# Kernel optimization log

Measured on AMD Instinct MI355X. Metric: run time of the kernel, lower is better.

The kernel has to match this reference:

```python
import jax, jax.numpy as jnp
import numpy as np

TOP_K = 2
SCALING = 16.0 / 8.0  # alpha / rank


def setup_inputs() -> dict:
    key = jax.random.key(0)
    ks = jax.random.split(key, 9)
    B, V, D, P = 32, 21, 512, 64
    IN, OUT, E, R, H = D * P, 96, 8, 8, 256
    return {
        "x": jax.random.normal(ks[0], (B, V, D, P), jnp.float32),
        "W_base": jax.random.normal(ks[1], (OUT, IN), jnp.float32) * (IN ** -0.5),
        "b_base": jax.random.normal(ks[2], (OUT,), jnp.float32) * 0.01,
        "W1": jax.random.normal(ks[3], (H, D), jnp.float32) * (D ** -0.5),
        "b1": jax.random.normal(ks[4], (H,), jnp.float32) * 0.01,
        "W2": jax.random.normal(ks[5], (E, H), jnp.float32) * (H ** -0.5),
        "b2": jax.random.normal(ks[6], (E,), jnp.float32) * 0.01,
        "lora_A": jax.random.normal(ks[7], (E, R, IN), jnp.float32) * (IN ** -0.5),
        "lora_B": jax.random.normal(ks[8], (E, OUT, R), jnp.float32) * (R ** -0.5),
    }


def reference(x, W_base, b_base, W1, b1, W2, b2, lora_A, lora_B):
    B, V, D, P = x.shape
    E = lora_A.shape[0]
    # FlattenHead: flatten last two dims, then linear (dropout is identity in eval)
    flat = x.reshape(B, V, D * P)                      # [B, V, IN]
    base_out = flat @ W_base.T + b_base                # [B, V, OUT]
    # Router: pool over n_vars then patch dim -> [B, D]
    pooled = x.mean(axis=1).mean(axis=-1)
    h = jax.nn.relu(pooled @ W1.T + b1)
    logits = h @ W2.T + b2                             # [B, E]
    probs = jax.nn.softmax(logits, axis=-1)
    topw, topi = jax.lax.top_k(probs, TOP_K)           # [B, K]
    topw = topw / jnp.clip(topw.sum(-1, keepdims=True), 1e-6)
    # All LoRA experts (matches original dense compute), then weighted combine
    temp = jnp.einsum("bvi,eri->ebvr", flat, lora_A)   # [E, B, V, R]
    delta = jnp.einsum("ebvr,eor->ebvo", temp, lora_B) * SCALING  # [E, B, V, OUT]
    # Scatter top-k weights into dense [B, E] then combine (top-k sparse combine)
    w_full = jnp.zeros((B, E), x.dtype).at[jnp.arange(B)[:, None], topi].add(topw)
    moe_delta = jnp.einsum("be,ebvo->bvo", w_full, delta)
    return base_out + moe_delta, probs
```

## Files before the change

kernel.cpp:

```cpp
#include <hip/hip_runtime.h>

#define B_DIM 32
#define V_DIM 21
#define D_DIM 512
#define P_DIM 64
#define M_TOTAL 672
#define K_TOTAL 32768
#define OUT_DIM 96
#define E_DIM 8
#define R_DIM 8
#define H_DIM 256
#define N_TOTAL 160
#define SCALING 2.0f
#define POOL_SCALE (1.0f / (V_DIM * (float)P_DIM))

#define BM 64
#define BK 32
#define KSPLIT 32
#define K_PER_SPLIT (K_TOTAL / KSPLIT)
#define CHUNKS (K_PER_SPLIT / BK)
#define SMN (M_TOTAL * N_TOTAL)
#define NMB 11
#define RC_ROWS 4

typedef __attribute__((ext_vector_type(4))) float floatx4;
typedef __attribute__((ext_vector_type(8))) short short8;

__device__ __forceinline__ unsigned short f2bf(float f) {
  union { float f; unsigned int u; } v; v.f = f;
  unsigned int u = v.u + (0x7FFFu + ((v.u >> 16) & 1u));
  return (unsigned short)(u >> 16);
}

__device__ __forceinline__ unsigned int cvt_pk_bf16(float lo, float hi) {
  unsigned int r;
  asm("v_cvt_pk_bf16_f32 %0, %1, %2" : "=v"(r) : "v"(lo), "v"(hi));
  return r;
}

__device__ __forceinline__ void gl_lds16(const void* g, void* l) {
  __builtin_amdgcn_global_load_lds(
      (const __attribute__((address_space(1))) void*)g,
      (__attribute__((address_space(3))) void*)l, 16, 0, 0);
}

__device__ __forceinline__ short8 as_s8(floatx4 v) {
  union { floatx4 f; short8 s; } u; u.f = v; return u.s;
}

__global__ __launch_bounds__(256)
void convW_kernel(const float* __restrict__ W_base, const float* __restrict__ lora_A,
                  short* __restrict__ Wb) {
  int gid = blockIdx.x * 256 + threadIdx.x;
  size_t base = (size_t)gid * 8;
  int row = (int)(base >> 15);
  int k = (int)(base & 32767);
  const float* src = (row < OUT_DIM) ? (W_base + ((size_t)row << 15) + k)
                                     : (lora_A + ((size_t)(row - OUT_DIM) << 15) + k);
  floatx4 v0 = ((const floatx4*)src)[0];
  floatx4 v1 = ((const floatx4*)src)[1];
  short8 sv;
  sv[0] = (short)f2bf(v0[0]); sv[1] = (short)f2bf(v0[1]);
  sv[2] = (short)f2bf(v0[2]); sv[3] = (short)f2bf(v0[3]);
  sv[4] = (short)f2bf(v1[0]); sv[5] = (short)f2bf(v1[1]);
  sv[6] = (short)f2bf(v1[2]); sv[7] = (short)f2bf(v1[3]);
  *(short8*)(Wb + base) = sv;
}

__global__ __launch_bounds__(256, 2)
void gemm_kernel(const float* __restrict__ x, const short* __restrict__ Wb,
                 float* __restrict__ P, float* __restrict__ pp) {
  __shared__ __attribute__((aligned(16))) short ldsB[4][N_TOTAL * BK];
  __shared__ float lds_pool[5 * 16];

  const int tid = threadIdx.x;
  const int bid = blockIdx.x;
  const int xcd = bid & 7;
  const int grp = bid >> 3;
  const int ky  = xcd + 8 * (grp / NMB);
  const int mb  = grp % NMB;
  const int m0 = mb * BM;
  const int kbase = ky * K_PER_SPLIT;
  const int lane = tid & 63;
  const int wave = tid >> 6;
  const int quad = lane >> 4;
  const int l16 = lane & 15;
  const int b_first = m0 / V_DIM;

  if (tid < 80) lds_pool[tid] = 0.0f;
  asm volatile("s_waitcnt lgkmcnt(0)" ::: "memory");

  const int arow_raw = m0 + wave * 16 + l16;
  const bool row_ok = (arow_raw < M_TOTAL);
  const int arow = row_ok ? arow_raw : (M_TOTAL - 1);
  const floatx4* aptr =
      (const floatx4*)(x + (size_t)arow * K_TOTAL + kbase + quad * 8);

  const short* srcB0; const short* srcB1; const short* srcB2 = Wb;
  int dstB0, dstB1, dstB2 = 0;
  {
    int idx = tid, pair = idx >> 3, s8 = idx & 7;
    srcB0 = Wb + (size_t)(2 * pair + (s8 >> 2)) * K_TOTAL + kbase + (s8 & 3) * 8;
    dstB0 = (tid & 192) << 3;
    idx = 256 + tid; pair = idx >> 3; s8 = idx & 7;
    srcB1 = Wb + (size_t)(2 * pair + (s8 >> 2)) * K_TOTAL + kbase + (s8 & 3) * 8;
    dstB1 = (256 + (tid & 192)) << 3;
    if (tid < 128) {
      idx = 512 + tid; pair = idx >> 3; s8 = idx & 7;
      srcB2 = Wb + (size_t)(2 * pair + (s8 >> 2)) * K_TOTAL + kbase + (s8 & 3) * 8;
      dstB2 = (512 + (tid & 192)) << 3;
    }
  }
  const unsigned baddr =
      (unsigned)(size_t)(__attribute__((address_space(3))) short*)&ldsB[0][0] +
      (unsigned)((l16 >> 1) * 128 + ((((l16 & 1) << 2) | quad) * 16));

#define ISSUE_B(c, bb)                                                        \
  {                                                                           \
    gl_lds16(srcB0 + (c) * BK, &ldsB[bb][dstB0]);                             \
    gl_lds16(srcB1 + (c) * BK, &ldsB[bb][dstB1]);                             \
    if (tid < 128) gl_lds16(srcB2 + (c) * BK, &ldsB[bb][dstB2]);              \
  }
#define WAITV(N) asm volatile("s_waitcnt vmcnt(" #N ")" ::: "memory")
#define SBAR __builtin_amdgcn_sched_barrier(0)

  floatx4 af[4][2];
  floatx4 acc[10];
  #pragma unroll
  for (int nt = 0; nt < 10; ++nt) acc[nt] = (floatx4)(0.0f);
  floatx4 paccv = (floatx4)(0.0f);

  ISSUE_B(0, 0); SBAR;
  af[0][0] = aptr[0];  af[0][1] = aptr[1];  SBAR;
  ISSUE_B(1, 1); SBAR;
  af[1][0] = aptr[8];  af[1][1] = aptr[9];  SBAR;
  ISSUE_B(2, 2); SBAR;
  af[2][0] = aptr[16]; af[2][1] = aptr[17];
  af[3][0] = aptr[24]; af[3][1] = aptr[25];

  #pragma unroll
  for (int c = 0; c < CHUNKS; ++c) {
    const int bb = c & 3;
    if (c <= CHUNKS - 4)      { if (wave < 2) WAITV(12); else WAITV(10); }
    else if (c == CHUNKS - 3) { if (wave < 2) WAITV(10); else WAITV(8); }
    else if (c == CHUNKS - 2) { if (wave < 2) WAITV(5);  else WAITV(4); }
    else                      { WAITV(0); }
    SBAR;
    __builtin_amdgcn_s_barrier();
    SBAR;
    if (c + 3 < CHUNKS) ISSUE_B(c + 3, (c + 3) & 3);
    SBAR;
    floatx4 f0 = af[bb][0], f1 = af[bb][1];
    union { short8 s; unsigned int u[4]; } av;
    av.u[0] = cvt_pk_bf16(f0[0], f0[1]);
    av.u[1] = cvt_pk_bf16(f0[2], f0[3]);
    av.u[2] = cvt_pk_bf16(f1[0], f1[1]);
    av.u[3] = cvt_pk_bf16(f1[2], f1[3]);
    paccv += f0 + f1;
    if (c & 1) {
      float h = (paccv[0] + paccv[1]) + (paccv[2] + paccv[3]);
      h += __shfl_down(h, 32);
      h += __shfl_down(h, 16);
      if (lane < 16 && row_ok)
        atomicAdd(&lds_pool[(arow / V_DIM - b_first) * 16 + (c >> 1)], h);
      paccv = (floatx4)(0.0f);
    }
    if (c + 4 < CHUNKS) {
      af[bb][0] = aptr[(c + 4) * 8];
      af[bb][1] = aptr[(c + 4) * 8 + 1];
    }
    const unsigned ba = baddr + (unsigned)(bb * (N_TOTAL * BK * 2));
    floatx4 b0, b1, b2, b3, b4, b5, b6, b7, b8, b9;
    asm volatile("ds_read_b128 %0, %1 offset:0"    : "=&v"(b0) : "v"(ba));
    asm volatile("ds_read_b128 %0, %1 offset:1024" : "=&v"(b1) : "v"(ba));
    asm volatile("ds_read_b128 %0, %1 offset:2048" : "=&v"(b2) : "v"(ba));
    asm volatile("ds_read_b128 %0, %1 offset:3072" : "=&v"(b3) : "v"(ba));
    asm volatile("ds_read_b128 %0, %1 offset:4096" : "=&v"(b4) : "v"(ba));
    asm volatile("ds_read_b128 %0, %1 offset:5120" : "=&v"(b5) : "v"(ba));
    asm volatile("ds_read_b128 %0, %1 offset:6144" : "=&v"(b6) : "v"(ba));
    asm volatile("ds_read_b128 %0, %1 offset:7168" : "=&v"(b7) : "v"(ba));
    asm volatile("ds_read_b128 %0, %1 offset:8192" : "=&v"(b8) : "v"(ba));
    asm volatile("ds_read_b128 %0, %1 offset:9216" : "=&v"(b9) : "v"(ba));
    asm volatile("s_waitcnt lgkmcnt(0)" ::: "memory");
    SBAR;
    acc[0] = __builtin_amdgcn_mfma_f32_16x16x32_bf16(av.s, as_s8(b0), acc[0], 0, 0, 0);
    acc[1] = __builtin_amdgcn_mfma_f32_16x16x32_bf16(av.s, as_s8(b1), acc[1], 0, 0, 0);
    acc[2] = __builtin_amdgcn_mfma_f32_16x16x32_bf16(av.s, as_s8(b2), acc[2], 0, 0, 0);
    acc[3] = __builtin_amdgcn_mfma_f32_16x16x32_bf16(av.s, as_s8(b3), acc[3], 0, 0, 0);
    acc[4] = __builtin_amdgcn_mfma_f32_16x16x32_bf16(av.s, as_s8(b4), acc[4], 0, 0, 0);
    acc[5] = __builtin_amdgcn_mfma_f32_16x16x32_bf16(av.s, as_s8(b5), acc[5], 0, 0, 0);
    acc[6] = __builtin_amdgcn_mfma_f32_16x16x32_bf16(av.s, as_s8(b6), acc[6], 0, 0, 0);
    acc[7] = __builtin_amdgcn_mfma_f32_16x16x32_bf16(av.s, as_s8(b7), acc[7], 0, 0, 0);
    acc[8] = __builtin_amdgcn_mfma_f32_16x16x32_bf16(av.s, as_s8(b8), acc[8], 0, 0, 0);
    acc[9] = __builtin_amdgcn_mfma_f32_16x16x32_bf16(av.s, as_s8(b9), acc[9], 0, 0, 0);
  }

  __syncthreads();

  {
    const int mrow = m0 + wave * 16 + quad * 4;
    float* Pp = P + (size_t)ky * SMN + (size_t)mrow * N_TOTAL + l16;
    #pragma unroll
    for (int r = 0; r < 4; ++r)
      if (mrow + r < M_TOTAL)
        #pragma unroll
        for (int nt = 0; nt < 10; ++nt)
          Pp[(size_t)r * N_TOTAL + nt * 16] = acc[nt][r];
  }

  if (tid < 80) {
    int bl = tid >> 4, dl = tid & 15;
    pp[((size_t)(mb * 5 + bl)) * D_DIM + ky * 16 + dl] = lds_pool[tid];
  }
}

__global__ __launch_bounds__(256)
void router_kernel(const float* __restrict__ pp, const float* __restrict__ W1,
                   const float* __restrict__ b1, const float* __restrict__ W2,
                   const float* __restrict__ b2, float* __restrict__ wfull,
                   float* __restrict__ probs_out) {
  __shared__ float sp[D_DIM];
  __shared__ float sh[H_DIM];
  __shared__ float slog[E_DIM];
  const int b = blockIdx.x;
  const int t = threadIdx.x;
  const int mb1 = (b * V_DIM) / BM;
  const int mb2 = (b * V_DIM + V_DIM - 1) / BM;
  const int bf1 = (mb1 * BM) / V_DIM;
  const int bf2 = (mb2 * BM) / V_DIM;
  const float* p1 = pp + (size_t)(mb1 * 5 + (b - bf1)) * D_DIM;
  const float* p2 = pp + (size_t)(mb2 * 5 + (b - bf2)) * D_DIM;
  for (int d = t; d < D_DIM; d += 256) {
    float v = p1[d];
    if (mb2 != mb1) v += p2[d];
    sp[d] = v * POOL_SCALE;
  }
  __syncthreads();
  float acc = b1[t];
  const float* w1r = W1 + (size_t)t * D_DIM;
  for (int d = 0; d < D_DIM; ++d) acc += sp[d] * w1r[d];
  sh[t] = fmaxf(acc, 0.0f);
  __syncthreads();
  if (t < E_DIM) {
    float a = b2[t];
    const float* w2r = W2 + t * H_DIM;
    for (int j = 0; j < H_DIM; ++j) a += sh[j] * w2r[j];
    slog[t] = a;
  }
  __syncthreads();
  if (t == 0) {
    float p[E_DIM];
    float mx = slog[0];
    for (int e = 1; e < E_DIM; ++e) mx = fmaxf(mx, slog[e]);
    float se = 0.0f;
    for (int e = 0; e < E_DIM; ++e) { p[e] = __expf(slog[e] - mx); se += p[e]; }
    float inv = 1.0f / se;
    for (int e = 0; e < E_DIM; ++e) { p[e] *= inv; probs_out[b * E_DIM + e] = p[e]; }
    int i0 = 0;
    for (int e = 1; e < E_DIM; ++e) if (p[e] > p[i0]) i0 = e;
    int i1 = (i0 == 0) ? 1 : 0;
    for (int e = 0; e < E_DIM; ++e) if (e != i0 && p[e] > p[i1]) i1 = e;
    float s2 = p[i0] + p[i1];
    float invs = 1.0f / fmaxf(s2, 1e-6f);
    for (int e = 0; e < E_DIM; ++e) {
      float w = 0.0f;
      if (e == i0) w += p[i0] * invs;
      if (e == i1) w += p[i1] * invs;
      wfull[b * E_DIM + e] = w;
    }
  }
}

__global__ __launch_bounds__(256)
void reduce_combine_kernel(const float* __restrict__ P, const float* __restrict__ b_base,
                           const float* __restrict__ lora_B, const float* __restrict__ wfull,
                           float* __restrict__ out) {
  __shared__ float sS[RC_ROWS * N_TOTAL];
  const int t = threadIdx.x;
  const int NF4 = RC_ROWS * N_TOTAL / 4;
  if (t < NF4) {
    const floatx4* P4 = (const floatx4*)P;
    size_t base = (size_t)blockIdx.x * NF4 + t;
    floatx4 a = (floatx4)(0.0f);
    #pragma unroll 8
    for (int k = 0; k < KSPLIT; ++k) a += P4[(size_t)k * (SMN / 4) + base];
    *(floatx4*)&sS[t * 4] = a;
  }
  __syncthreads();
  for (int i = t; i < RC_ROWS * OUT_DIM; i += 256) {
    int mr = i / OUT_DIM;
    int o = i - mr * OUT_DIM;
    int mm = blockIdx.x * RC_ROWS + mr;
    int b = mm / V_DIM;
    const float* srow = sS + mr * N_TOTAL;
    float res = srow[o] + b_base[o];
    float moe = 0.0f;
    #pragma unroll
    for (int e = 0; e < E_DIM; ++e) {
      float we = wfull[b * E_DIM + e];
      if (we != 0.0f) {
        const float* lb = lora_B + ((size_t)e * OUT_DIM + o) * R_DIM;
        float dd = 0.0f;
        #pragma unroll
        for (int r = 0; r < R_DIM; ++r) dd += srow[OUT_DIM + e * R_DIM + r] * lb[r];
        moe += we * dd;
      }
    }
    out[(size_t)mm * OUT_DIM + o] = res + SCALING * moe;
  }
}

extern "C" void kernel_launch(void* const* d_in, const int* in_sizes, int n_in,
                              void* d_out, int out_size, void* d_ws, size_t ws_size,
                              hipStream_t stream) {
  const float* x      = (const float*)d_in[0];
  const float* W_base = (const float*)d_in[1];
  const float* b_base = (const float*)d_in[2];
  const float* W1     = (const float*)d_in[3];
  const float* b1     = (const float*)d_in[4];
  const float* W2     = (const float*)d_in[5];
  const float* b2     = (const float*)d_in[6];
  const float* lora_A = (const float*)d_in[7];
  const float* lora_B = (const float*)d_in[8];
  float* out = (float*)d_out;

  float* ws    = (float*)d_ws;
  float* pp    = ws;
  float* wfull = ws + NMB * 5 * D_DIM;
  short* Wb    = (short*)(wfull + 256);
  float* P     = (float*)(Wb + (size_t)N_TOTAL * K_TOTAL);

  convW_kernel<<<(N_TOTAL * K_TOTAL / 8 + 255) / 256, 256, 0, stream>>>(
      W_base, lora_A, Wb);
  gemm_kernel<<<NMB * KSPLIT, 256, 0, stream>>>(x, Wb, P, pp);
  router_kernel<<<B_DIM, 256, 0, stream>>>(pp, W1, b1, W2, b2, wfull,
                                           out + (size_t)M_TOTAL * OUT_DIM);
  reduce_combine_kernel<<<M_TOTAL / RC_ROWS, 256, 0, stream>>>(
      P, b_base, lora_B, wfull, out);
}
```

Baseline: 214.6 us.

## Pre-swizzle bf16 weights into MFMA fragment order and load B directly to registers

The weight conversion kernel now writes bf16 weights in a layout matching the MFMA B-fragment order per K-split and chunk. This lets the GEMM drop the LDS staging, async global-to-LDS copies, per-chunk barriers and vmcnt choreography, and instead double-buffer B fragments in registers via direct global loads. The M tile grows from 64 to 96 rows (6 waves, 384 threads, 7 M-blocks), which divides 672 exactly and removes the row bounds checks. Each wave now fetches the full B tile itself, so global/L2 traffic for B rises, and register pressure increases with 20 short8 B buffers.

Result: slower. 219.7 us (+2.4%).

```diff
diff --git a/kernel.cpp b/kernel.cpp
--- a/kernel.cpp
+++ b/kernel.cpp
@@ -14,13 +14,13 @@
 #define SCALING 2.0f
 #define POOL_SCALE (1.0f / (V_DIM * (float)P_DIM))
 
-#define BM 64
+#define BM 96
 #define BK 32
 #define KSPLIT 32
 #define K_PER_SPLIT (K_TOTAL / KSPLIT)
 #define CHUNKS (K_PER_SPLIT / BK)
 #define SMN (M_TOTAL * N_TOTAL)
-#define NMB 11
+#define NMB 7
 #define RC_ROWS 4
 
 typedef __attribute__((ext_vector_type(4))) float floatx4;
@@ -36,16 +36,6 @@
   unsigned int r;
   asm("v_cvt_pk_bf16_f32 %0, %1, %2" : "=v"(r) : "v"(lo), "v"(hi));
   return r;
-}
-
-__device__ __forceinline__ void gl_lds16(const void* g, void* l) {
-  __builtin_amdgcn_global_load_lds(
-      (const __attribute__((address_space(1))) void*)g,
-      (__attribute__((address_space(3))) void*)l, 16, 0, 0);
-}
-
-__device__ __forceinline__ short8 as_s8(floatx4 v) {
-  union { floatx4 f; short8 s; } u; u.f = v; return u.s;
 }
 
 __global__ __launch_bounds__(256)
@@ -64,14 +54,16 @@
   sv[2] = (short)f2bf(v0[2]); sv[3] = (short)f2bf(v0[3]);
   sv[4] = (short)f2bf(v1[0]); sv[5] = (short)f2bf(v1[1]);
   sv[6] = (short)f2bf(v1[2]); sv[7] = (short)f2bf(v1[3]);
-  *(short8*)(Wb + base) = sv;
-}
-
-__global__ __launch_bounds__(256, 2)
+  int ky = k >> 10, c = (k >> 5) & 31, quad = (k >> 3) & 3;
+  int nt = row >> 4, l16 = row & 15;
+  size_t off = ((size_t)(ky * 32 + c) * 10 + nt) * 512 + l16 * 32 + quad * 8;
+  *(short8*)(Wb + off) = sv;
+}
+
+__global__ __launch_bounds__(384)
 void gemm_kernel(const float* __restrict__ x, const short* __restrict__ Wb,
                  float* __restrict__ P, float* __restrict__ pp) {
-  __shared__ __attribute__((aligned(16))) short ldsB[4][N_TOTAL * BK];
-  __shared__ float lds_pool[5 * 16];
+  __shared__ float lds_pool[6 * 16];
 
   const int tid = threadIdx.x;
   const int bid = blockIdx.x;
@@ -87,70 +79,42 @@
   const int l16 = lane & 15;
   const int b_first = m0 / V_DIM;
 
-  if (tid < 80) lds_pool[tid] = 0.0f;
+  if (tid < 96) lds_pool[tid] = 0.0f;
   asm volatile("s_waitcnt lgkmcnt(0)" ::: "memory");
-
-  const int arow_raw = m0 + wave * 16 + l16;
-  const bool row_ok = (arow_raw < M_TOTAL);
-  const int arow = row_ok ? arow_raw : (M_TOTAL - 1);
+  __builtin_amdgcn_s_barrier();
+
+  const int arow = m0 + wave * 16 + l16;
   const floatx4* aptr =
       (const floatx4*)(x + (size_t)arow * K_TOTAL + kbase + quad * 8);
-
-  const short* srcB0; const short* srcB1; const short* srcB2 = Wb;
-  int dstB0, dstB1, dstB2 = 0;
-  {
-    int idx = tid, pair = idx >> 3, s8 = idx & 7;
-    srcB0 = Wb + (size_t)(2 * pair + (s8 >> 2)) * K_TOTAL + kbase + (s8 & 3) * 8;
-    dstB0 = (tid & 192) << 3;
-    idx = 256 + tid; pair = idx >> 3; s8 = idx & 7;
-    srcB1 = Wb + (size_t)(2 * pair + (s8 >> 2)) * K_TOTAL + kbase + (s8 & 3) * 8;
-    dstB1 = (256 + (tid & 192)) << 3;
-    if (tid < 128) {
-      idx = 512 + tid; pair = idx >> 3; s8 = idx & 7;
-      srcB2 = Wb + (size_t)(2 * pair + (s8 >> 2)) * K_TOTAL + kbase + (s8 & 3) * 8;
-      dstB2 = (512 + (tid & 192)) << 3;
-    }
-  }
-  const unsigned baddr =
-      (unsigned)(size_t)(__attribute__((address_space(3))) short*)&ldsB[0][0] +
-      (unsigned)((l16 >> 1) * 128 + ((((l16 & 1) << 2) | quad) * 16));
-
-#define ISSUE_B(c, bb)                                                        \
-  {                                                                           \
-    gl_lds16(srcB0 + (c) * BK, &ldsB[bb][dstB0]);                             \
-    gl_lds16(srcB1 + (c) * BK, &ldsB[bb][dstB1]);                             \
-    if (tid < 128) gl_lds16(srcB2 + (c) * BK, &ldsB[bb][dstB2]);              \
-  }
-#define WAITV(N) asm volatile("s_waitcnt vmcnt(" #N ")" ::: "memory")
-#define SBAR __builtin_amdgcn_sched_barrier(0)
-
+  const short* bbase = Wb + (size_t)ky * (CHUNKS * 5120) + l16 * 32 + quad * 8;
+  const int pool_idx = (arow / V_DIM - b_first) * 16;
+
+  short8 bf[2][10];
   floatx4 af[4][2];
   floatx4 acc[10];
   #pragma unroll
   for (int nt = 0; nt < 10; ++nt) acc[nt] = (floatx4)(0.0f);
   floatx4 paccv = (floatx4)(0.0f);
 
-  ISSUE_B(0, 0); SBAR;
-  af[0][0] = aptr[0];  af[0][1] = aptr[1];  SBAR;
-  ISSUE_B(1, 1); SBAR;
-  af[1][0] = aptr[8];  af[1][1] = aptr[9];  SBAR;
-  ISSUE_B(2, 2); SBAR;
+  #pragma unroll
+  for (int nt = 0; nt < 10; ++nt)
+    bf[0][nt] = *(const short8*)(bbase + nt * 512);
+  #pragma unroll
+  for (int nt = 0; nt < 10; ++nt)
+    bf[1][nt] = *(const short8*)(bbase + 5120 + nt * 512);
+  af[0][0] = aptr[0];  af[0][1] = aptr[1];
+  af[1][0] = aptr[8];  af[1][1] = aptr[9];
   af[2][0] = aptr[16]; af[2][1] = aptr[17];
   af[3][0] = aptr[24]; af[3][1] = aptr[25];
 
   #pragma unroll
   for (int c = 0; c < CHUNKS; ++c) {
-    const int bb = c & 3;
-    if (c <= CHUNKS - 4)      { if (wave < 2) WAITV(12); else WAITV(10); }
-    else if (c == CHUNKS - 3) { if (wave < 2) WAITV(10); else WAITV(8); }
-    else if (c == CHUNKS - 2) { if (wave < 2) WAITV(5);  else WAITV(4); }
-    else                      { WAITV(0); }
-    SBAR;
-    __builtin_amdgcn_s_barrier();
-    SBAR;
-    if (c + 3 < CHUNKS) ISSUE_B(c + 3, (c + 3) & 3);
-    SBAR;
-    floatx4 f0 = af[bb][0], f1 = af[bb][1];
+    const int ab = c & 3, bb = c & 1;
+    floatx4 f0 = af[ab][0], f1 = af[ab][1];
+    if (c + 4 < CHUNKS) {
+      af[ab][0] = aptr[(c + 4) * 8];
+      af[ab][1] = aptr[(c + 4) * 8 + 1];
+    }
     union { short8 s; unsigned int u[4]; } av;
     av.u[0] = cvt_pk_bf16(f0[0], f0[1]);
     av.u[1] = cvt_pk_bf16(f0[2], f0[3]);
@@ -161,38 +125,19 @@
       float h = (paccv[0] + paccv[1]) + (paccv[2] + paccv[3]);
       h += __shfl_down(h, 32);
       h += __shfl_down(h, 16);
-      if (lane < 16 && row_ok)
-        atomicAdd(&lds_pool[(arow / V_DIM - b_first) * 16 + (c >> 1)], h);
+      if (lane < 16)
+        atomicAdd(&lds_pool[pool_idx + (c >> 1)], h);
       paccv = (floatx4)(0.0f);
     }
-    if (c + 4 < CHUNKS) {
-      af[bb][0] = aptr[(c + 4) * 8];
-      af[bb][1] = aptr[(c + 4) * 8 + 1];
-    }
-    const unsigned ba = baddr + (unsigned)(bb * (N_TOTAL * BK * 2));
-    floatx4 b0, b1, b2, b3, b4, b5, b6, b7, b8, b9;
-    asm volatile("ds_read_b128 %0, %1 offset:0"    : "=&v"(b0) : "v"(ba));
-    asm volatile("ds_read_b128 %0, %1 offset:1024" : "=&v"(b1) : "v"(ba));
-    asm volatile("ds_read_b128 %0, %1 offset:2048" : "=&v"(b2) : "v"(ba));
-    asm volatile("ds_read_b128 %0, %1 offset:3072" : "=&v"(b3) : "v"(ba));
-    asm volatile("ds_read_b128 %0, %1 offset:4096" : "=&v"(b4) : "v"(ba));
-    asm volatile("ds_read_b128 %0, %1 offset:5120" : "=&v"(b5) : "v"(ba));
-    asm volatile("ds_read_b128 %0, %1 offset:6144" : "=&v"(b6) : "v"(ba));
-    asm volatile("ds_read_b128 %0, %1 offset:7168" : "=&v"(b7) : "v"(ba));
-    asm volatile("ds_read_b128 %0, %1 offset:8192" : "=&v"(b8) : "v"(ba));
-    asm volatile("ds_read_b128 %0, %1 offset:9216" : "=&v"(b9) : "v"(ba));
-    asm volatile("s_waitcnt lgkmcnt(0)" ::: "memory");
-    SBAR;
-    acc[0] = __builtin_amdgcn_mfma_f32_16x16x32_bf16(av.s, as_s8(b0), acc[0], 0, 0, 0);
-    acc[1] = __builtin_amdgcn_mfma_f32_16x16x32_bf16(av.s, as_s8(b1), acc[1], 0, 0, 0);
-    acc[2] = __builtin_amdgcn_mfma_f32_16x16x32_bf16(av.s, as_s8(b2), acc[2], 0, 0, 0);
-    acc[3] = __builtin_amdgcn_mfma_f32_16x16x32_bf16(av.s, as_s8(b3), acc[3], 0, 0, 0);
-    acc[4] = __builtin_amdgcn_mfma_f32_16x16x32_bf16(av.s, as_s8(b4), acc[4], 0, 0, 0);
-    acc[5] = __builtin_amdgcn_mfma_f32_16x16x32_bf16(av.s, as_s8(b5), acc[5], 0, 0, 0);
-    acc[6] = __builtin_amdgcn_mfma_f32_16x16x32_bf16(av.s, as_s8(b6), acc[6], 0, 0, 0);
-    acc[7] = __builtin_amdgcn_mfma_f32_16x16x32_bf16(av.s, as_s8(b7), acc[7], 0, 0, 0);
-    acc[8] = __builtin_amdgcn_mfma_f32_16x16x32_bf16(av.s, as_s8(b8), acc[8], 0, 0, 0);
-    acc[9] = __builtin_amdgcn_mfma_f32_16x16x32_bf16(av.s, as_s8(b9), acc[9], 0, 0, 0);
+    #pragma unroll
+    for (int nt = 0; nt < 10; ++nt)
+      acc[nt] = __builtin_amdgcn_mfma_f32_16x16x32_bf16(av.s, bf[bb][nt],
+                                                        acc[nt], 0, 0, 0);
+    if (c + 2 < CHUNKS) {
+      #pragma unroll
+      for (int nt = 0; nt < 10; ++nt)
+        bf[bb][nt] = *(const short8*)(bbase + (c + 2) * 5120 + nt * 512);
+    }
   }
 
   __syncthreads();
@@ -202,15 +147,14 @@
     float* Pp = P + (size_t)ky * SMN + (size_t)mrow * N_TOTAL + l16;
     #pragma unroll
     for (int r = 0; r < 4; ++r)
-      if (mrow + r < M_TOTAL)
-        #pragma unroll
-        for (int nt = 0; nt < 10; ++nt)
-          Pp[(size_t)r * N_TOTAL + nt * 16] = acc[nt][r];
-  }
-
-  if (tid < 80) {
+      #pragma unroll
+      for (int nt = 0; nt < 10; ++nt)
+        Pp[(size_t)r * N_TOTAL + nt * 16] = acc[nt][r];
+  }
+
+  if (tid < 96) {
     int bl = tid >> 4, dl = tid & 15;
-    pp[((size_t)(mb * 5 + bl)) * D_DIM + ky * 16 + dl] = lds_pool[tid];
+    pp[((size_t)(mb * 6 + bl)) * D_DIM + ky * 16 + dl] = lds_pool[tid];
   }
 }
 
@@ -228,8 +172,8 @@
   const int mb2 = (b * V_DIM + V_DIM - 1) / BM;
   const int bf1 = (mb1 * BM) / V_DIM;
   const int bf2 = (mb2 * BM) / V_DIM;
-  const float* p1 = pp + (size_t)(mb1 * 5 + (b - bf1)) * D_DIM;
-  const float* p2 = pp + (size_t)(mb2 * 5 + (b - bf2)) * D_DIM;
+  const float* p1 = pp + (size_t)(mb1 * 6 + (b - bf1)) * D_DIM;
+  const float* p2 = pp + (size_t)(mb2 * 6 + (b - bf2)) * D_DIM;
   for (int d = t; d < D_DIM; d += 256) {
     float v = p1[d];
     if (mb2 != mb1) v += p2[d];
@@ -326,13 +270,13 @@
 
   float* ws    = (float*)d_ws;
   float* pp    = ws;
-  float* wfull = ws + NMB * 5 * D_DIM;
+  float* wfull = ws + NMB * 6 * D_DIM;
   short* Wb    = (short*)(wfull + 256);
   float* P     = (float*)(Wb + (size_t)N_TOTAL * K_TOTAL);
 
   convW_kernel<<<(N_TOTAL * K_TOTAL / 8 + 255) / 256, 256, 0, stream>>>(
       W_base, lora_A, Wb);
-  gemm_kernel<<<NMB * KSPLIT, 256, 0, stream>>>(x, Wb, P, pp);
+  gemm_kernel<<<NMB * KSPLIT, 384, 0, stream>>>(x, Wb, P, pp);
   router_kernel<<<B_DIM, 256, 0, stream>>>(pp, W1, b1, W2, b2, wfull,
                                            out + (size_t)M_TOTAL * OUT_DIM);
   reduce_combine_kernel<<<M_TOTAL / RC_ROWS, 256, 0, stream>>>(
```
